# Performance work log

Hardware: AMD Instinct MI355X
Metric: run time of the kernel (lower is better)

Reference implementation:

```python
import jax, jax.numpy as jnp
import numpy as np

N = 100000
E = 1600000
IN_DIM, HID, OUT, DW = 128, 64, 32, 64
NUM_GCN, NUM_LBL = 2, 10


def glorot(key, shape):
    lim = float(np.sqrt(6.0 / (shape[0] + shape[1])))
    return jax.random.uniform(key, shape, jnp.float32, -lim, lim)


def setup_inputs() -> dict:
    key = jax.random.key(0)
    ks = jax.random.split(key, 12)
    x = jax.random.normal(ks[0], (N, IN_DIM), jnp.float32)
    y = jax.random.uniform(ks[1], (N, OUT), jnp.float32)
    edge_index = jax.random.randint(ks[2], (2, E), 0, N, jnp.int32)
    deep_walk_emb = jax.random.normal(ks[3], (N, DW), jnp.float32)
    label_input_mask = jax.random.bernoulli(ks[4], 0.5, (N,))
    W_gcn0 = glorot(ks[5], (IN_DIM, HID))
    b_gcn0 = jnp.zeros((HID,), jnp.float32)
    W_gcn1 = glorot(ks[6], (HID, HID))
    b_gcn1 = jnp.zeros((HID,), jnp.float32)
    W_label = jax.vmap(glorot, in_axes=(0, None))(jax.random.split(ks[7], NUM_LBL), (OUT, OUT))
    b_label = jnp.zeros((NUM_LBL, OUT), jnp.float32)
    W_fuse = glorot(ks[8], (HID + OUT + DW, OUT))
    b_fuse = jnp.zeros((OUT,), jnp.float32)
    return {"x": x, "y": y, "edge_index": edge_index, "deep_walk_emb": deep_walk_emb,
            "label_input_mask": label_input_mask,
            "W_gcn0": W_gcn0, "b_gcn0": b_gcn0, "W_gcn1": W_gcn1, "b_gcn1": b_gcn1,
            "W_label": W_label, "b_label": b_label, "W_fuse": W_fuse, "b_fuse": b_fuse}


def _gcn_norm(edge_index):
    # symmetric GCN normalization with self-loops (PyG GCNConv default)
    src, dst = edge_index[0], edge_index[1]
    deg = jax.ops.segment_sum(jnp.ones((E,), jnp.float32), dst, num_segments=N) + 1.0
    dinv = jax.lax.rsqrt(deg)
    norm = dinv[src] * dinv[dst]          # per-edge coefficient
    inv_deg = dinv * dinv                 # self-loop coefficient 1/deg
    return src, dst, norm, inv_deg


def _gcn_conv(x, W, b, src, dst, norm, inv_deg):
    h = x @ W                              # [N, F_out] linear first (PyG order)
    agg = jax.ops.segment_sum(norm[:, None] * h[src], dst, num_segments=N)
    return agg + inv_deg[:, None] * h + b


def reference(x, y, edge_index, deep_walk_emb, label_input_mask,
              W_gcn0, b_gcn0, W_gcn1, b_gcn1, W_label, b_label, W_fuse, b_fuse):
    src, dst, norm, inv_deg = _gcn_norm(edge_index)
    # feature propagation
    h = _gcn_conv(x, W_gcn0, b_gcn0, src, dst, norm, inv_deg)
    h = _gcn_conv(h, W_gcn1, b_gcn1, src, dst, norm, inv_deg)
    # label propagation with masked overwrite of known labels each step
    xl = y
    for j in range(NUM_LBL):
        xl = _gcn_conv(xl, W_label[j], b_label[j], src, dst, norm, inv_deg)
        xl = jnp.where(label_input_mask[:, None], y, xl)
    fused = jnp.concatenate((h, xl, deep_walk_emb), axis=1)
    out = fused @ W_fuse + b_fuse
    return jax.nn.sigmoid(out)
```

## Files before the change

kernel.cpp:

```cpp
#include <hip/hip_runtime.h>
#include <math.h>

static constexpr int IN_DIM  = 128;
static constexpr int HID     = 64;
static constexpr int OUT_F   = 32;
static constexpr int NUM_LBL = 10;


__global__ void count_deg_k(const int* __restrict__ dst, int* __restrict__ deg, int E) {
    int e = blockIdx.x * 256 + threadIdx.x;
    if (e < E) atomicAdd(&deg[dst[e]], 1);
}

__global__ void dinv_k(const int* __restrict__ deg, float* __restrict__ dinv, int n) {
    int i = blockIdx.x * 256 + threadIdx.x;
    if (i < n) dinv[i] = rsqrtf((float)deg[i] + 1.0f);
}

__global__ void scan_partials_k(const int* __restrict__ deg, int* __restrict__ partials, int n) {
    __shared__ int s[256];
    int i = blockIdx.x * 256 + threadIdx.x;
    s[threadIdx.x] = (i < n) ? deg[i] : 0;
    __syncthreads();
    for (int st = 128; st > 0; st >>= 1) {
        if (threadIdx.x < st) s[threadIdx.x] += s[threadIdx.x + st];
        __syncthreads();
    }
    if (threadIdx.x == 0) partials[blockIdx.x] = s[0];
}

__global__ void scan_top_k(int* __restrict__ partials, int nb) {
    __shared__ int s[512];
    int t = threadIdx.x;
    int v = (t < nb) ? partials[t] : 0;
    s[t] = v;
    __syncthreads();
    for (int off = 1; off < 512; off <<= 1) {
        int x = (t >= off) ? s[t - off] : 0;
        __syncthreads();
        s[t] += x;
        __syncthreads();
    }
    if (t < nb) partials[t] = s[t] - v;
}

__global__ void scan_final_k(const int* __restrict__ deg, const int* __restrict__ partials,
                             int* __restrict__ row_ptr, int* __restrict__ cursor, int n, int E) {
    __shared__ int s[256];
    int t = threadIdx.x;
    int i = blockIdx.x * 256 + t;
    int v = (i < n) ? deg[i] : 0;
    s[t] = v;
    __syncthreads();
    for (int off = 1; off < 256; off <<= 1) {
        int x = (t >= off) ? s[t - off] : 0;
        __syncthreads();
        s[t] += x;
        __syncthreads();
    }
    int excl = s[t] - v + partials[blockIdx.x];
    if (i < n) { row_ptr[i] = excl; cursor[i] = excl; }
    if (i == 0) row_ptr[n] = E;
}

__global__ void fill_csr_k(const int* __restrict__ src, const int* __restrict__ dst,
                           int* __restrict__ cursor, int* __restrict__ col, int E) {
    int e = blockIdx.x * 256 + threadIdx.x;
    if (e < E) {
        int pos = atomicAdd(&cursor[dst[e]], 1);
        col[pos] = src[e];
    }
}


template<int K, int F>
__global__ void linear_scale_k(const float* __restrict__ x, const float* __restrict__ W,
                               const float* __restrict__ dinv, float* __restrict__ g, int n) {
    __shared__ float Ws[K * F];
    for (int idx = threadIdx.x; idx < K * F; idx += 256) Ws[idx] = W[idx];
    __syncthreads();
    constexpr int RPB = 256 / F;
    int col = threadIdx.x % F;
    int row = blockIdx.x * RPB + threadIdx.x / F;
    if (row >= n) return;
    const float4* x4 = (const float4*)(x + (size_t)row * K);
    float acc = 0.f;
#pragma unroll
    for (int k4 = 0; k4 < K / 4; ++k4) {
        float4 xv = x4[k4];
        acc += xv.x * Ws[(4 * k4 + 0) * F + col];
        acc += xv.y * Ws[(4 * k4 + 1) * F + col];
        acc += xv.z * Ws[(4 * k4 + 2) * F + col];
        acc += xv.w * Ws[(4 * k4 + 3) * F + col];
    }
    g[(size_t)row * F + col] = dinv[row] * acc;
}

template<int F, bool MASK>
__global__ void gcn_gather_k(const float* __restrict__ g, const int* __restrict__ row_ptr,
                             const int* __restrict__ col, const float* __restrict__ dinv,
                             const float* __restrict__ bias, const int* __restrict__ mask,
                             const float* __restrict__ y, float* __restrict__ out, int n) {
    constexpr int NPW = 64 / F;
    int lane = threadIdx.x & 63;
    int wid  = threadIdx.x >> 6;
    int f = lane % F;
    int i = (blockIdx.x * 4 + wid) * NPW + lane / F;
    if (i >= n) return;
    int beg = row_ptr[i], end = row_ptr[i + 1];
    float acc = 0.f;
    int p = beg;
    for (; p + 4 <= end; p += 4) {
        int s0 = col[p], s1 = col[p + 1], s2 = col[p + 2], s3 = col[p + 3];
        acc += g[(size_t)s0 * F + f];
        acc += g[(size_t)s1 * F + f];
        acc += g[(size_t)s2 * F + f];
        acc += g[(size_t)s3 * F + f];
    }
    for (; p < end; ++p) acc += g[(size_t)col[p] * F + f];
    float v = dinv[i] * (acc + g[(size_t)i * F + f]) + bias[f];
    if (MASK) { if (mask[i]) v = y[(size_t)i * F + f]; }
    out[(size_t)i * F + f] = v;
}

__global__ void fuse_k(const float* __restrict__ h, const float* __restrict__ xl,
                       const float* __restrict__ dw, const float* __restrict__ Wf,
                       const float* __restrict__ bf, float* __restrict__ out, int n) {
    __shared__ float Ws[160 * 32];
    for (int idx = threadIdx.x; idx < 160 * 32; idx += 256) Ws[idx] = Wf[idx];
    __syncthreads();
    int col = threadIdx.x & 31;
    int row = blockIdx.x * 8 + (threadIdx.x >> 5);
    if (row >= n) return;
    float acc = bf[col];
    const float4* h4 = (const float4*)(h + (size_t)row * 64);
#pragma unroll
    for (int k4 = 0; k4 < 16; ++k4) {
        float4 v = h4[k4]; int kb = k4 * 4;
        acc += v.x * Ws[(kb + 0) * 32 + col];
        acc += v.y * Ws[(kb + 1) * 32 + col];
        acc += v.z * Ws[(kb + 2) * 32 + col];
        acc += v.w * Ws[(kb + 3) * 32 + col];
    }
    const float4* x4 = (const float4*)(xl + (size_t)row * 32);
#pragma unroll
    for (int k4 = 0; k4 < 8; ++k4) {
        float4 v = x4[k4]; int kb = 64 + k4 * 4;
        acc += v.x * Ws[(kb + 0) * 32 + col];
        acc += v.y * Ws[(kb + 1) * 32 + col];
        acc += v.z * Ws[(kb + 2) * 32 + col];
        acc += v.w * Ws[(kb + 3) * 32 + col];
    }
    const float4* d4 = (const float4*)(dw + (size_t)row * 64);
#pragma unroll
    for (int k4 = 0; k4 < 16; ++k4) {
        float4 v = d4[k4]; int kb = 96 + k4 * 4;
        acc += v.x * Ws[(kb + 0) * 32 + col];
        acc += v.y * Ws[(kb + 1) * 32 + col];
        acc += v.z * Ws[(kb + 2) * 32 + col];
        acc += v.w * Ws[(kb + 3) * 32 + col];
    }
    out[(size_t)row * 32 + col] = 1.0f / (1.0f + __expf(-acc));
}


extern "C" void kernel_launch(void* const* d_in, const int* in_sizes, int n_in,
                              void* d_out, int out_size, void* d_ws, size_t ws_size,
                              hipStream_t stream) {
    const float* x    = (const float*)d_in[0];
    const float* y    = (const float*)d_in[1];
    const int*   ei   = (const int*)  d_in[2];
    const float* dw   = (const float*)d_in[3];
    const int*   mask = (const int*)  d_in[4];
    const float* Wg0  = (const float*)d_in[5];
    const float* bg0  = (const float*)d_in[6];
    const float* Wg1  = (const float*)d_in[7];
    const float* bg1  = (const float*)d_in[8];
    const float* Wl   = (const float*)d_in[9];
    const float* bl   = (const float*)d_in[10];
    const float* Wf   = (const float*)d_in[11];
    const float* bf   = (const float*)d_in[12];
    float* out = (float*)d_out;

    const int N = in_sizes[0] / IN_DIM;
    const int E = in_sizes[2] / 2;
    const int* src = ei;
    const int* dst = ei + E;

    char* w = (char*)d_ws;
    size_t off = 0;
    auto alloc = [&](size_t bytes) -> char* {
        off = (off + 255) & ~(size_t)255;
        char* p = w + off; off += bytes; return p;
    };
    float* dinv   = (float*)alloc((size_t)N * 4);
    int*   deg    = (int*)  alloc((size_t)N * 4);
    int*   rowp   = (int*)  alloc((size_t)(N + 1) * 4);
    int*   cursor = (int*)  alloc((size_t)N * 4);
    int*   parts  = (int*)  alloc(512 * 4);
    int*   colx   = (int*)  alloc((size_t)E * 4);
    float* gbuf   = (float*)alloc((size_t)N * HID * 4);
    float* hbuf   = (float*)alloc((size_t)N * HID * 4);
    float* xlA    = (float*)alloc((size_t)N * OUT_F * 4);
    float* xlB    = (float*)alloc((size_t)N * OUT_F * 4);
    (void)ws_size; (void)n_in; (void)out_size;

    const int nbN = (N + 255) / 256;
    const int nbE = (E + 255) / 256;

    hipMemsetAsync(deg, 0, (size_t)N * 4, stream);
    count_deg_k<<<nbE, 256, 0, stream>>>(dst, deg, E);
    dinv_k<<<nbN, 256, 0, stream>>>(deg, dinv, N);
    scan_partials_k<<<nbN, 256, 0, stream>>>(deg, parts, N);
    scan_top_k<<<1, 512, 0, stream>>>(parts, nbN);
    scan_final_k<<<nbN, 256, 0, stream>>>(deg, parts, rowp, cursor, N, E);
    fill_csr_k<<<nbE, 256, 0, stream>>>(src, dst, cursor, colx, E);

    linear_scale_k<IN_DIM, HID><<<(N + 3) / 4, 256, 0, stream>>>(x, Wg0, dinv, gbuf, N);
    gcn_gather_k<HID, false><<<(N + 3) / 4, 256, 0, stream>>>(gbuf, rowp, colx, dinv, bg0, nullptr, nullptr, hbuf, N);
    linear_scale_k<HID, HID><<<(N + 3) / 4, 256, 0, stream>>>(hbuf, Wg1, dinv, gbuf, N);
    gcn_gather_k<HID, false><<<(N + 3) / 4, 256, 0, stream>>>(gbuf, rowp, colx, dinv, bg1, nullptr, nullptr, hbuf, N);

    const float* xl_cur = y;
    for (int j = 0; j < NUM_LBL; ++j) {
        float* xl_out = (j & 1) ? xlB : xlA;
        linear_scale_k<OUT_F, OUT_F><<<(N + 7) / 8, 256, 0, stream>>>(xl_cur, Wl + (size_t)j * OUT_F * OUT_F, dinv, gbuf, N);
        gcn_gather_k<OUT_F, true><<<(N + 7) / 8, 256, 0, stream>>>(gbuf, rowp, colx, dinv, bl + (size_t)j * OUT_F, mask, y, xl_out, N);
        xl_cur = xl_out;
    }

    fuse_k<<<(N + 7) / 8, 256, 0, stream>>>(hbuf, xl_cur, dw, Wf, bf, out, N);
}
```

Baseline: 1.433 ms.

## Store scaled features in bf16 and split neighbor lists across lanes in gather

The intermediate scaled features g are now stored as packed bf16 pairs, halving gather traffic. The gather kernel assigns one node per wavefront and spreads its edges across lane groups, reducing the partial sums with shuffles. The linear and fuse kernels compute two output columns per thread and process 64-row chunks per block, reusing the shared-memory weight load. The bf16 rounding of g adds precision loss in the propagated features, and on low-degree nodes many lanes may sit idle.

```diff
diff --git a/kernel.cpp b/kernel.cpp
--- a/kernel.cpp
+++ b/kernel.cpp
@@ -5,6 +5,16 @@
 static constexpr int HID     = 64;
 static constexpr int OUT_F   = 32;
 static constexpr int NUM_LBL = 10;
+
+__device__ __forceinline__ unsigned int f2bf_lo(float f) {
+    unsigned int u = __float_as_uint(f);
+    return (u + 0x7fffu + ((u >> 16) & 1u)) >> 16;
+}
+__device__ __forceinline__ unsigned int pack_bf2(float a, float b) {
+    return f2bf_lo(a) | (f2bf_lo(b) << 16);
+}
+__device__ __forceinline__ float bf2f_lo(unsigned int v) { return __uint_as_float(v << 16); }
+__device__ __forceinline__ float bf2f_hi(unsigned int v) { return __uint_as_float(v & 0xffff0000u); }
 
 
 __global__ void count_deg_k(const int* __restrict__ dst, int* __restrict__ deg, int E) {
@@ -75,92 +85,136 @@
 
 template<int K, int F>
 __global__ void linear_scale_k(const float* __restrict__ x, const float* __restrict__ W,
-                               const float* __restrict__ dinv, float* __restrict__ g, int n) {
+                               const float* __restrict__ dinv,
+                               unsigned int* __restrict__ g, int n) {
+    constexpr int L = F / 2;
+    constexpr int RPP = 256 / L;
+    constexpr int CHUNK = 64;
     __shared__ float Ws[K * F];
-    for (int idx = threadIdx.x; idx < K * F; idx += 256) Ws[idx] = W[idx];
-    __syncthreads();
-    constexpr int RPB = 256 / F;
-    int col = threadIdx.x % F;
-    int row = blockIdx.x * RPB + threadIdx.x / F;
-    if (row >= n) return;
-    const float4* x4 = (const float4*)(x + (size_t)row * K);
-    float acc = 0.f;
-#pragma unroll
-    for (int k4 = 0; k4 < K / 4; ++k4) {
-        float4 xv = x4[k4];
-        acc += xv.x * Ws[(4 * k4 + 0) * F + col];
-        acc += xv.y * Ws[(4 * k4 + 1) * F + col];
-        acc += xv.z * Ws[(4 * k4 + 2) * F + col];
-        acc += xv.w * Ws[(4 * k4 + 3) * F + col];
-    }
-    g[(size_t)row * F + col] = dinv[row] * acc;
+    {
+        const float4* W4 = (const float4*)W;
+        float4* Ws4 = (float4*)Ws;
+        for (int idx = threadIdx.x; idx < K * F / 4; idx += 256) Ws4[idx] = W4[idx];
+    }
+    __syncthreads();
+    const float2* Ws2 = (const float2*)Ws;
+    int c2 = threadIdx.x % L;
+    int rend = min(n, (int)(blockIdx.x * CHUNK + CHUNK));
+    for (int r = blockIdx.x * CHUNK + threadIdx.x / L; r < rend; r += RPP) {
+        const float4* x4 = (const float4*)(x + (size_t)r * K);
+        float2 acc = {0.f, 0.f};
+#pragma unroll
+        for (int k4 = 0; k4 < K / 4; ++k4) {
+            float4 xv = x4[k4];
+            float2 w0 = Ws2[(4 * k4 + 0) * L + c2];
+            float2 w1 = Ws2[(4 * k4 + 1) * L + c2];
+            float2 w2 = Ws2[(4 * k4 + 2) * L + c2];
+            float2 w3 = Ws2[(4 * k4 + 3) * L + c2];
+            acc.x += xv.x * w0.x; acc.y += xv.x * w0.y;
+            acc.x += xv.y * w1.x; acc.y += xv.y * w1.y;
+            acc.x += xv.z * w2.x; acc.y += xv.z * w2.y;
+            acc.x += xv.w * w3.x; acc.y += xv.w * w3.y;
+        }
+        float di = dinv[r];
+        g[(size_t)r * L + c2] = pack_bf2(di * acc.x, di * acc.y);
+    }
 }
 
 template<int F, bool MASK>
-__global__ void gcn_gather_k(const float* __restrict__ g, const int* __restrict__ row_ptr,
+__global__ void gcn_gather_k(const unsigned int* __restrict__ g, const int* __restrict__ row_ptr,
                              const int* __restrict__ col, const float* __restrict__ dinv,
                              const float* __restrict__ bias, const int* __restrict__ mask,
                              const float* __restrict__ y, float* __restrict__ out, int n) {
-    constexpr int NPW = 64 / F;
+    constexpr int L = F / 2;
+    constexpr int S = 64 / L;
     int lane = threadIdx.x & 63;
     int wid  = threadIdx.x >> 6;
-    int f = lane % F;
-    int i = (blockIdx.x * 4 + wid) * NPW + lane / F;
+    int c2 = lane % L;
+    int sp = lane / L;
+    int i = blockIdx.x * 4 + wid;
     if (i >= n) return;
     int beg = row_ptr[i], end = row_ptr[i + 1];
-    float acc = 0.f;
-    int p = beg;
-    for (; p + 4 <= end; p += 4) {
-        int s0 = col[p], s1 = col[p + 1], s2 = col[p + 2], s3 = col[p + 3];
-        acc += g[(size_t)s0 * F + f];
-        acc += g[(size_t)s1 * F + f];
-        acc += g[(size_t)s2 * F + f];
-        acc += g[(size_t)s3 * F + f];
-    }
-    for (; p < end; ++p) acc += g[(size_t)col[p] * F + f];
-    float v = dinv[i] * (acc + g[(size_t)i * F + f]) + bias[f];
-    if (MASK) { if (mask[i]) v = y[(size_t)i * F + f]; }
-    out[(size_t)i * F + f] = v;
+    float2 acc = {0.f, 0.f};
+    for (int p = beg + sp; p < end; p += S) {
+        int s = col[p];
+        unsigned int v = g[(size_t)s * L + c2];
+        acc.x += bf2f_lo(v);
+        acc.y += bf2f_hi(v);
+    }
+#pragma unroll
+    for (int m = 32; m >= L; m >>= 1) {
+        acc.x += __shfl_xor(acc.x, m);
+        acc.y += __shfl_xor(acc.y, m);
+    }
+    if (sp == 0) {
+        unsigned int gi = g[(size_t)i * L + c2];
+        float di = dinv[i];
+        float2 v;
+        v.x = di * (acc.x + bf2f_lo(gi)) + bias[2 * c2];
+        v.y = di * (acc.y + bf2f_hi(gi)) + bias[2 * c2 + 1];
+        if (MASK) {
+            if (mask[i]) v = ((const float2*)y)[(size_t)i * L + c2];
+        }
+        ((float2*)out)[(size_t)i * L + c2] = v;
+    }
 }
 
 __global__ void fuse_k(const float* __restrict__ h, const float* __restrict__ xl,
                        const float* __restrict__ dw, const float* __restrict__ Wf,
                        const float* __restrict__ bf, float* __restrict__ out, int n) {
+    constexpr int L = 16;
+    constexpr int RPP = 16;
+    constexpr int CHUNK = 64;
     __shared__ float Ws[160 * 32];
-    for (int idx = threadIdx.x; idx < 160 * 32; idx += 256) Ws[idx] = Wf[idx];
-    __syncthreads();
-    int col = threadIdx.x & 31;
-    int row = blockIdx.x * 8 + (threadIdx.x >> 5);
-    if (row >= n) return;
-    float acc = bf[col];
-    const float4* h4 = (const float4*)(h + (size_t)row * 64);
-#pragma unroll
-    for (int k4 = 0; k4 < 16; ++k4) {
-        float4 v = h4[k4]; int kb = k4 * 4;
-        acc += v.x * Ws[(kb + 0) * 32 + col];
-        acc += v.y * Ws[(kb + 1) * 32 + col];
-        acc += v.z * Ws[(kb + 2) * 32 + col];
-        acc += v.w * Ws[(kb + 3) * 32 + col];
-    }
-    const float4* x4 = (const float4*)(xl + (size_t)row * 32);
-#pragma unroll
-    for (int k4 = 0; k4 < 8; ++k4) {
-        float4 v = x4[k4]; int kb = 64 + k4 * 4;
-        acc += v.x * Ws[(kb + 0) * 32 + col];
-        acc += v.y * Ws[(kb + 1) * 32 + col];
-        acc += v.z * Ws[(kb + 2) * 32 + col];
-        acc += v.w * Ws[(kb + 3) * 32 + col];
-    }
-    const float4* d4 = (const float4*)(dw + (size_t)row * 64);
-#pragma unroll
-    for (int k4 = 0; k4 < 16; ++k4) {
-        float4 v = d4[k4]; int kb = 96 + k4 * 4;
-        acc += v.x * Ws[(kb + 0) * 32 + col];
-        acc += v.y * Ws[(kb + 1) * 32 + col];
-        acc += v.z * Ws[(kb + 2) * 32 + col];
-        acc += v.w * Ws[(kb + 3) * 32 + col];
-    }
-    out[(size_t)row * 32 + col] = 1.0f / (1.0f + __expf(-acc));
+    {
+        const float4* W4 = (const float4*)Wf;
+        float4* Ws4 = (float4*)Ws;
+        for (int idx = threadIdx.x; idx < 160 * 32 / 4; idx += 256) Ws4[idx] = W4[idx];
+    }
+    __syncthreads();
+    const float2* Ws2 = (const float2*)Ws;
+    int c2 = threadIdx.x % L;
+    int rend = min(n, (int)(blockIdx.x * CHUNK + CHUNK));
+    for (int r = blockIdx.x * CHUNK + threadIdx.x / L; r < rend; r += RPP) {
+        float2 acc = {bf[2 * c2], bf[2 * c2 + 1]};
+        const float4* h4 = (const float4*)(h + (size_t)r * 64);
+#pragma unroll
+        for (int k4 = 0; k4 < 16; ++k4) {
+            float4 v = h4[k4]; int kb = k4 * 4;
+            float2 w0 = Ws2[(kb + 0) * L + c2], w1 = Ws2[(kb + 1) * L + c2];
+            float2 w2 = Ws2[(kb + 2) * L + c2], w3 = Ws2[(kb + 3) * L + c2];
+            acc.x += v.x * w0.x; acc.y += v.x * w0.y;
+            acc.x += v.y * w1.x; acc.y += v.y * w1.y;
+            acc.x += v.z * w2.x; acc.y += v.z * w2.y;
+            acc.x += v.w * w3.x; acc.y += v.w * w3.y;
+        }
+        const float4* x4 = (const float4*)(xl + (size_t)r * 32);
+#pragma unroll
+        for (int k4 = 0; k4 < 8; ++k4) {
+            float4 v = x4[k4]; int kb = 64 + k4 * 4;
+            float2 w0 = Ws2[(kb + 0) * L + c2], w1 = Ws2[(kb + 1) * L + c2];
+            float2 w2 = Ws2[(kb + 2) * L + c2], w3 = Ws2[(kb + 3) * L + c2];
+            acc.x += v.x * w0.x; acc.y += v.x * w0.y;
+            acc.x += v.y * w1.x; acc.y += v.y * w1.y;
+            acc.x += v.z * w2.x; acc.y += v.z * w2.y;
+            acc.x += v.w * w3.x; acc.y += v.w * w3.y;
+        }
+        const float4* d4 = (const float4*)(dw + (size_t)r * 64);
+#pragma unroll
+        for (int k4 = 0; k4 < 16; ++k4) {
+            float4 v = d4[k4]; int kb = 96 + k4 * 4;
+            float2 w0 = Ws2[(kb + 0) * L + c2], w1 = Ws2[(kb + 1) * L + c2];
+            float2 w2 = Ws2[(kb + 2) * L + c2], w3 = Ws2[(kb + 3) * L + c2];
+            acc.x += v.x * w0.x; acc.y += v.x * w0.y;
+            acc.x += v.y * w1.x; acc.y += v.y * w1.y;
+            acc.x += v.z * w2.x; acc.y += v.z * w2.y;
+            acc.x += v.w * w3.x; acc.y += v.w * w3.y;
+        }
+        float2 o;
+        o.x = 1.0f / (1.0f + __expf(-acc.x));
+        o.y = 1.0f / (1.0f + __expf(-acc.y));
+        ((float2*)out)[(size_t)r * L + c2] = o;
+    }
 }
 
 
@@ -199,7 +253,7 @@
     int*   cursor = (int*)  alloc((size_t)N * 4);
     int*   parts  = (int*)  alloc(512 * 4);
     int*   colx   = (int*)  alloc((size_t)E * 4);
-    float* gbuf   = (float*)alloc((size_t)N * HID * 4);
+    unsigned int* gbuf = (unsigned int*)alloc((size_t)N * (HID / 2) * 4);
     float* hbuf   = (float*)alloc((size_t)N * HID * 4);
     float* xlA    = (float*)alloc((size_t)N * OUT_F * 4);
     float* xlB    = (float*)alloc((size_t)N * OUT_F * 4);
@@ -207,8 +261,10 @@
 
     const int nbN = (N + 255) / 256;
     const int nbE = (E + 255) / 256;
-
-    hipMemsetAsync(deg, 0, (size_t)N * 4, stream);
+    const int nbC = (N + 63) / 64;
+    const int nbG = (N + 3) / 4;
+
+    (void)hipMemsetAsync(deg, 0, (size_t)N * 4, stream);
     count_deg_k<<<nbE, 256, 0, stream>>>(dst, deg, E);
     dinv_k<<<nbN, 256, 0, stream>>>(deg, dinv, N);
     scan_partials_k<<<nbN, 256, 0, stream>>>(deg, parts, N);
@@ -216,18 +272,18 @@
     scan_final_k<<<nbN, 256, 0, stream>>>(deg, parts, rowp, cursor, N, E);
     fill_csr_k<<<nbE, 256, 0, stream>>>(src, dst, cursor, colx, E);
 
-    linear_scale_k<IN_DIM, HID><<<(N + 3) / 4, 256, 0, stream>>>(x, Wg0, dinv, gbuf, N);
-    gcn_gather_k<HID, false><<<(N + 3) / 4, 256, 0, stream>>>(gbuf, rowp, colx, dinv, bg0, nullptr, nullptr, hbuf, N);
-    linear_scale_k<HID, HID><<<(N + 3) / 4, 256, 0, stream>>>(hbuf, Wg1, dinv, gbuf, N);
-    gcn_gather_k<HID, false><<<(N + 3) / 4, 256, 0, stream>>>(gbuf, rowp, colx, dinv, bg1, nullptr, nullptr, hbuf, N);
+    linear_scale_k<IN_DIM, HID><<<nbC, 256, 0, stream>>>(x, Wg0, dinv, gbuf, N);
+    gcn_gather_k<HID, false><<<nbG, 256, 0, stream>>>(gbuf, rowp, colx, dinv, bg0, nullptr, nullptr, hbuf, N);
+    linear_scale_k<HID, HID><<<nbC, 256, 0, stream>>>(hbuf, Wg1, dinv, gbuf, N);
+    gcn_gather_k<HID, false><<<nbG, 256, 0, stream>>>(gbuf, rowp, colx, dinv, bg1, nullptr, nullptr, hbuf, N);
 
     const float* xl_cur = y;
     for (int j = 0; j < NUM_LBL; ++j) {
         float* xl_out = (j & 1) ? xlB : xlA;
-        linear_scale_k<OUT_F, OUT_F><<<(N + 7) / 8, 256, 0, stream>>>(xl_cur, Wl + (size_t)j * OUT_F * OUT_F, dinv, gbuf, N);
-        gcn_gather_k<OUT_F, true><<<(N + 7) / 8, 256, 0, stream>>>(gbuf, rowp, colx, dinv, bl + (size_t)j * OUT_F, mask, y, xl_out, N);
+        linear_scale_k<OUT_F, OUT_F><<<nbC, 256, 0, stream>>>(xl_cur, Wl + (size_t)j * OUT_F * OUT_F, dinv, gbuf, N);
+        gcn_gather_k<OUT_F, true><<<nbG, 256, 0, stream>>>(gbuf, rowp, colx, dinv, bl + (size_t)j * OUT_F, mask, y, xl_out, N);
         xl_cur = xl_out;
     }
 
-    fuse_k<<<(N + 7) / 8, 256, 0, stream>>>(hbuf, xl_cur, dw, Wf, bf, out, N);
-}
+    fuse_k<<<nbC, 256, 0, stream>>>(hbuf, xl_cur, dw, Wf, bf, out, N);
+}
```

Result: slower. 3.381 ms (+135.9%).
